# Kernel tuning notes

Hardware: AMD Instinct MI355X
Metric: run time of the kernel (lower is better)

The kernel has to match this reference:

```python
import jax, jax.numpy as jnp
import numpy as np

GRID_SIZE = 5
SPLINE_ORDER = 3

def _grid(in_features, dtype):
    # efficient-KAN default grid over [-1, 1], extended by spline_order knots each side
    h = 2.0 / GRID_SIZE
    g = jnp.arange(-SPLINE_ORDER, GRID_SIZE + SPLINE_ORDER + 1, dtype=dtype) * h - 1.0
    return jnp.broadcast_to(g, (in_features, g.shape[0]))  # (in, G+2k+1)

def _b_splines(x, grid):
    # x: (..., in) -> bases: (..., in, G+k) via Cox-de Boor recursion
    xk = x[..., None]
    bases = ((xk >= grid[:, :-1]) & (xk < grid[:, 1:])).astype(x.dtype)
    for k in range(1, SPLINE_ORDER + 1):
        left = (xk - grid[:, :-(k + 1)]) / (grid[:, k:-1] - grid[:, :-(k + 1)]) * bases[..., :-1]
        right = (grid[:, k + 1:] - xk) / (grid[:, k + 1:] - grid[:, 1:-k]) * bases[..., 1:]
        bases = left + right
    return bases

def _kan_linear(x, base_w, spline_w, scaler):
    # base branch: SiLU(x) @ W_base^T ; spline branch: einsum over B-spline basis
    grid = _grid(base_w.shape[1], x.dtype)
    bases = _b_splines(x, grid)                      # (..., in, G+k)
    scaled = spline_w * scaler[..., None]            # (out, in, G+k)
    base_out = jax.nn.silu(x) @ base_w.T
    spline_out = jnp.einsum('...ig,oig->...o', bases, scaled)
    return base_out + spline_out

def setup_inputs() -> dict:
    key = jax.random.key(0)
    ks = jax.random.split(key, 11)
    B, N, C, O = 2, 256, 64, 64
    GK = GRID_SIZE + SPLINE_ORDER
    return {
        'x': jax.random.normal(ks[0], (B, N, C), jnp.float32),
        'adj': jax.random.randint(ks[1], (B, N, N), 0, 2, jnp.int32),
        'fw_base': jax.random.normal(ks[2], (1, C), jnp.float32) * 0.1,
        'fw_spline': jax.random.normal(ks[3], (1, C, GK), jnp.float32) * 0.1,
        'fw_scaler': jax.random.normal(ks[4], (1, C), jnp.float32) * 0.1,
        'mw_base': jax.random.normal(ks[5], (O, C), jnp.float32) * 0.1,
        'mw_spline': jax.random.normal(ks[6], (O, C, GK), jnp.float32) * 0.1,
        'mw_scaler': jax.random.normal(ks[7], (O, C), jnp.float32) * 0.1,
        'uw_base': jax.random.normal(ks[8], (O, C + O), jnp.float32) * 0.1,
        'uw_spline': jax.random.normal(ks[9], (O, C + O, GK), jnp.float32) * 0.1,
        'uw_scaler': jax.random.normal(ks[10], (O, C + O), jnp.float32) * 0.1,
    }

def reference(x, adj, fw_base, fw_spline, fw_scaler, mw_base, mw_spline, mw_scaler, uw_base, uw_spline, uw_scaler):
    # r_ij = h_i - h_j : (B, N, N, C)
    r_ij = x[:, :, None, :] - x[:, None, :, :]
    energy = _kan_linear(r_ij, fw_base, fw_spline, fw_scaler)[..., 0]  # (B, N, N)
    energy = jnp.where(adj == 0, jnp.asarray(-1e9, energy.dtype), energy)
    alpha = jax.nn.softmax(energy, axis=-1)
    msg_val = _kan_linear(x, mw_base, mw_spline, mw_scaler)            # (B, N, O)
    aggr = jnp.einsum('bij,bjo->bio', alpha, msg_val)
    combined = jnp.concatenate([x, aggr], axis=-1)
    return _kan_linear(combined, uw_base, uw_spline, uw_scaler)
```

## Files before the change

### kernel.cpp

```cpp
#include <hip/hip_runtime.h>
#include <math.h>

#define NB 256
#define CH 64
#define OUTF 64
#define GK 8
#define UIN 128
#define KM (CH * 9)
#define KM4 (KM / 4)
#define KU (UIN * 9)
#define KU4 (KU / 4)

#define WS_MSG 0
#define WS_W2M 32768
#define WS_W2U 69632

__device__ __forceinline__ float silu(float v) {
    return v * __builtin_amdgcn_rcpf(1.0f + __expf(-v));
}

__device__ __forceinline__ void spline4(float r, int& d, float4& v) {
    float p = fmaf(r, 2.5f, 5.5f);
    float fd = floorf(p);
    d = (int)fd;
    float u = p - fd;
    if ((unsigned)d > 10u) d = 11;
    float um = 1.0f - u;
    float u2 = u * u, u3 = u2 * u;
    const float k6 = 1.0f / 6.0f;
    v.x = um * um * um * k6;
    v.y = (3.0f * u3 - 6.0f * u2 + 4.0f) * k6;
    v.z = (-3.0f * u3 + 3.0f * u2 + 3.0f * u + 1.0f) * k6;
    v.w = u3 * k6;
}

__global__ __launch_bounds__(256) void prep_kernel(
    const float* __restrict__ mwb, const float* __restrict__ mws,
    const float* __restrict__ mwsc,
    const float* __restrict__ uwb, const float* __restrict__ uws,
    const float* __restrict__ uwsc,
    float* __restrict__ ws) {
    int t = blockIdx.x * 256 + threadIdx.x;
    if (t < KM4 * OUTF) {
        int k4 = t >> 6, o = t & 63;
        float4 v;
#pragma unroll
        for (int kk = 0; kk < 4; ++kk) {
            int k = k4 * 4 + kk, c = k / 9, g = k - c * 9;
            ((float*)&v)[kk] = (g < 8)
                ? mws[(o * CH + c) * GK + g] * mwsc[o * CH + c]
                : mwb[o * CH + c];
        }
        ((float4*)(ws + WS_W2M))[t] = v;
        return;
    }
    int t2 = t - KM4 * OUTF;
    if (t2 < KU4 * OUTF) {
        int k4 = t2 >> 6, o = t2 & 63;
        float4 v;
#pragma unroll
        for (int kk = 0; kk < 4; ++kk) {
            int k = k4 * 4 + kk, c = k / 9, g = k - c * 9;
            ((float*)&v)[kk] = (g < 8)
                ? uws[(o * UIN + c) * GK + g] * uwsc[o * UIN + c]
                : uwb[o * UIN + c];
        }
        ((float4*)(ws + WS_W2U))[t2] = v;
    }
}

__global__ __launch_bounds__(256) void msg_kernel(
    const float* __restrict__ x, const float* __restrict__ w2m,
    float* __restrict__ msg) {
    const int row = blockIdx.x, tid = threadIdx.x;
    __shared__ __align__(16) float F[KM];
    __shared__ float part[4][OUTF];

    if (tid < CH) {
        float v = x[row * CH + tid];
#pragma unroll
        for (int g = 0; g < 8; ++g) F[tid * 9 + g] = 0.0f;
        F[tid * 9 + 8] = silu(v);
        int d; float4 vv; spline4(v, d, vv);
#pragma unroll
        for (int k = 0; k < 4; ++k) {
            int m = d - 3 + k;
            if ((unsigned)m < 8u) F[tid * 9 + m] = ((const float*)&vv)[k];
        }
    }
    __syncthreads();

    const int o = tid & 63, w = tid >> 6;
    const float4* W = (const float4*)w2m;
    const float4* Fv = (const float4*)F;
    float acc = 0.0f;
#pragma unroll 4
    for (int k4 = w * 36; k4 < w * 36 + 36; ++k4) {
        float4 f = Fv[k4];
        float4 wt = W[k4 * 64 + o];
        acc += f.x * wt.x + f.y * wt.y + f.z * wt.z + f.w * wt.w;
    }
    part[w][o] = acc;
    __syncthreads();
    if (tid < OUTF)
        msg[row * OUTF + tid] =
            part[0][tid] + part[1][tid] + part[2][tid] + part[3][tid];
}

__global__ __launch_bounds__(256, 2) void gat_kernel(
    const float* __restrict__ x,
    const int* __restrict__ adj,
    const float* __restrict__ fwb, const float* __restrict__ fws,
    const float* __restrict__ fwsc,
    const float* __restrict__ w2u,
    const float* __restrict__ msg,
    float* __restrict__ out) {
    const int b = blockIdx.x >> 8;
    const int i = blockIdx.x & 255;
    const int tid = threadIdx.x;

    __shared__ float4 cpad[CH][16];
    __shared__ float4 xi4[16];
    __shared__ float4 fb4[16];
    __shared__ float alpha[NB];
    __shared__ float comb[UIN];
    __shared__ __align__(16) float Fu[KU];
    __shared__ float4 part4[16][16];
    __shared__ float part[4][OUTF];
    __shared__ float wred[4];

    float4 xj[16];
    {
        const float4* xrow = (const float4*)(x + (b * NB + tid) * CH);
#pragma unroll
        for (int c4 = 0; c4 < 16; ++c4) xj[c4] = xrow[c4];
    }

    if (tid < 16) {
        float4 v = ((const float4*)(x + (b * NB + i) * CH))[tid];
        xi4[tid] = v;
        fb4[tid] = ((const float4*)fwb)[tid];
        ((float4*)comb)[tid] = v;
    }
#pragma unroll
    for (int e = tid; e < CH * 16; e += 256) {
        int c = e >> 4, dd = e & 15;
        float4 cf = make_float4(0.f, 0.f, 0.f, 0.f);
        if (dd <= 10) {
            float sc = fwsc[c];
            float w0 = 0.f, w1 = 0.f, w2 = 0.f, w3 = 0.f;
            int m0 = dd - 3;
            if ((unsigned)(m0 + 0) < 8u) w0 = fws[c * GK + m0 + 0] * sc;
            if ((unsigned)(m0 + 1) < 8u) w1 = fws[c * GK + m0 + 1] * sc;
            if ((unsigned)(m0 + 2) < 8u) w2 = fws[c * GK + m0 + 2] * sc;
            if ((unsigned)(m0 + 3) < 8u) w3 = fws[c * GK + m0 + 3] * sc;
            cf.x = (w0 + 4.0f * w1 + w2) * (1.0f / 6.0f);
            cf.y = (w2 - w0) * 0.5f;
            cf.z = (w0 - 2.0f * w1 + w2) * 0.5f;
            cf.w = (w3 - w0 + 3.0f * (w1 - w2)) * (1.0f / 6.0f);
        }
        cpad[c][dd] = cf;
    }
    __syncthreads();

    float e = 0.0f;
#pragma unroll
    for (int c4 = 0; c4 < 16; ++c4) {
        float4 xiv = xi4[c4];
        float4 fbv = fb4[c4];
        float4 xjv = xj[c4];
#pragma unroll
        for (int q = 0; q < 4; ++q) {
            float r = ((const float*)&xiv)[q] - ((const float*)&xjv)[q];
            float pp = fmaf(r, 2.5f, 5.5f);
            float fd = floorf(pp);
            int d = (int)fd;
            float u = pp - fd;
            if ((unsigned)d > 10u) d = 11;
            float4 cf = cpad[c4 * 4 + q][d];
            float t = fmaf(u, cf.w, cf.z);
            t = fmaf(u, t, cf.y);
            t = fmaf(u, t, cf.x);
            e += fmaf(silu(r), ((const float*)&fbv)[q], t);
        }
    }
    if (adj[(b * NB + i) * NB + tid] == 0) e = -1e9f;

    float mx = e;
#pragma unroll
    for (int off = 32; off > 0; off >>= 1)
        mx = fmaxf(mx, __shfl_xor(mx, off, 64));
    if ((tid & 63) == 0) wred[tid >> 6] = mx;
    __syncthreads();
    mx = fmaxf(fmaxf(wred[0], wred[1]), fmaxf(wred[2], wred[3]));
    float pexp = __expf(e - mx);
    float sw = pexp;
#pragma unroll
    for (int off = 32; off > 0; off >>= 1)
        sw += __shfl_xor(sw, off, 64);
    __syncthreads();
    if ((tid & 63) == 0) wred[tid >> 6] = sw;
    __syncthreads();
    float denom = wred[0] + wred[1] + wred[2] + wred[3];
    alpha[tid] = pexp * __builtin_amdgcn_rcpf(denom);
    __syncthreads();

    {
        const int o4 = tid & 15, seg = tid >> 4;
        const float4* msgb4 = (const float4*)(msg + (b * NB + seg * 16) * OUTF);
        float4 a = make_float4(0.f, 0.f, 0.f, 0.f);
#pragma unroll
        for (int jj = 0; jj < 16; ++jj) {
            float al = alpha[seg * 16 + jj];
            float4 mv = msgb4[jj * 16 + o4];
            a.x = fmaf(al, mv.x, a.x);
            a.y = fmaf(al, mv.y, a.y);
            a.z = fmaf(al, mv.z, a.z);
            a.w = fmaf(al, mv.w, a.w);
        }
        part4[seg][o4] = a;
    }
    __syncthreads();
    if (tid < OUTF) {
        const float* p = (const float*)part4;
        float s = 0.0f;
#pragma unroll
        for (int sg = 0; sg < 16; ++sg) s += p[sg * 64 + tid];
        comb[CH + tid] = s;
    }
    __syncthreads();

    if (tid < UIN) {
        float v = comb[tid];
#pragma unroll
        for (int g = 0; g < 8; ++g) Fu[tid * 9 + g] = 0.0f;
        Fu[tid * 9 + 8] = silu(v);
        int d; float4 vv; spline4(v, d, vv);
#pragma unroll
        for (int k = 0; k < 4; ++k) {
            int m = d - 3 + k;
            if ((unsigned)m < 8u) Fu[tid * 9 + m] = ((const float*)&vv)[k];
        }
    }
    __syncthreads();

    {
        const int o = tid & 63, w = tid >> 6;
        const float4* W = (const float4*)w2u;
        const float4* Fv = (const float4*)Fu;
        float acc = 0.0f;
#pragma unroll 4
        for (int k4 = w * 72; k4 < w * 72 + 72; ++k4) {
            float4 f = Fv[k4];
            float4 wt = W[k4 * 64 + o];
            acc += f.x * wt.x + f.y * wt.y + f.z * wt.z + f.w * wt.w;
        }
        part[w][o] = acc;
    }
    __syncthreads();
    if (tid < OUTF)
        out[(b * NB + i) * OUTF + tid] =
            part[0][tid] + part[1][tid] + part[2][tid] + part[3][tid];
}

extern "C" void kernel_launch(void* const* d_in, const int* in_sizes, int n_in,
                              void* d_out, int out_size, void* d_ws, size_t ws_size,
                              hipStream_t stream) {
    const float* x     = (const float*)d_in[0];
    const int*   adj   = (const int*)d_in[1];
    const float* fwb   = (const float*)d_in[2];
    const float* fws   = (const float*)d_in[3];
    const float* fwsc  = (const float*)d_in[4];
    const float* mwb   = (const float*)d_in[5];
    const float* mws   = (const float*)d_in[6];
    const float* mwsc  = (const float*)d_in[7];
    const float* uwb   = (const float*)d_in[8];
    const float* uws   = (const float*)d_in[9];
    const float* uwsc  = (const float*)d_in[10];
    float* out = (float*)d_out;
    float* ws = (float*)d_ws;

    const int BN = in_sizes[0] / CH;

    const int prep_threads = KM4 * OUTF + KU4 * OUTF;
    prep_kernel<<<(prep_threads + 255) / 256, 256, 0, stream>>>(
        mwb, mws, mwsc, uwb, uws, uwsc, ws);
    msg_kernel<<<BN, 256, 0, stream>>>(x, ws + WS_W2M, ws + WS_MSG);
    gat_kernel<<<BN, 256, 0, stream>>>(x, adj, fwb, fws, fwsc,
                                       ws + WS_W2U, ws + WS_MSG, out);
}
```

Measured before the change: 99.39 us.

## Process two query rows per block and precompute spline coefficient table in prep

Each msg and gat block now handles two rows, so the loaded xj neighbor rows, msg values, and w2u/w2m weight streams are reused across two outputs instead of being refetched per row. The cubic spline coefficient table for the energy KAN is computed once in the prep kernel and copied from workspace rather than rebuilt by every block. This halves the grid size (256 blocks for 512 rows) and raises register and shared-memory use per block, which may reduce occupancy and latency hiding.

```diff
diff --git a/kernel.cpp b/kernel.cpp
--- a/kernel.cpp
+++ b/kernel.cpp
@@ -14,6 +14,7 @@
 #define WS_MSG 0
 #define WS_W2M 32768
 #define WS_W2U 69632
+#define WS_CPAD 143360
 
 __device__ __forceinline__ float silu(float v) {
     return v * __builtin_amdgcn_rcpf(1.0f + __expf(-v));
@@ -39,6 +40,7 @@
     const float* __restrict__ mwsc,
     const float* __restrict__ uwb, const float* __restrict__ uws,
     const float* __restrict__ uwsc,
+    const float* __restrict__ fws, const float* __restrict__ fwsc,
     float* __restrict__ ws) {
     int t = blockIdx.x * 256 + threadIdx.x;
     if (t < KM4 * OUTF) {
@@ -66,85 +68,11 @@
                 : uwb[o * UIN + c];
         }
         ((float4*)(ws + WS_W2U))[t2] = v;
-    }
-}
-
-__global__ __launch_bounds__(256) void msg_kernel(
-    const float* __restrict__ x, const float* __restrict__ w2m,
-    float* __restrict__ msg) {
-    const int row = blockIdx.x, tid = threadIdx.x;
-    __shared__ __align__(16) float F[KM];
-    __shared__ float part[4][OUTF];
-
-    if (tid < CH) {
-        float v = x[row * CH + tid];
-#pragma unroll
-        for (int g = 0; g < 8; ++g) F[tid * 9 + g] = 0.0f;
-        F[tid * 9 + 8] = silu(v);
-        int d; float4 vv; spline4(v, d, vv);
-#pragma unroll
-        for (int k = 0; k < 4; ++k) {
-            int m = d - 3 + k;
-            if ((unsigned)m < 8u) F[tid * 9 + m] = ((const float*)&vv)[k];
-        }
-    }
-    __syncthreads();
-
-    const int o = tid & 63, w = tid >> 6;
-    const float4* W = (const float4*)w2m;
-    const float4* Fv = (const float4*)F;
-    float acc = 0.0f;
-#pragma unroll 4
-    for (int k4 = w * 36; k4 < w * 36 + 36; ++k4) {
-        float4 f = Fv[k4];
-        float4 wt = W[k4 * 64 + o];
-        acc += f.x * wt.x + f.y * wt.y + f.z * wt.z + f.w * wt.w;
-    }
-    part[w][o] = acc;
-    __syncthreads();
-    if (tid < OUTF)
-        msg[row * OUTF + tid] =
-            part[0][tid] + part[1][tid] + part[2][tid] + part[3][tid];
-}
-
-__global__ __launch_bounds__(256, 2) void gat_kernel(
-    const float* __restrict__ x,
-    const int* __restrict__ adj,
-    const float* __restrict__ fwb, const float* __restrict__ fws,
-    const float* __restrict__ fwsc,
-    const float* __restrict__ w2u,
-    const float* __restrict__ msg,
-    float* __restrict__ out) {
-    const int b = blockIdx.x >> 8;
-    const int i = blockIdx.x & 255;
-    const int tid = threadIdx.x;
-
-    __shared__ float4 cpad[CH][16];
-    __shared__ float4 xi4[16];
-    __shared__ float4 fb4[16];
-    __shared__ float alpha[NB];
-    __shared__ float comb[UIN];
-    __shared__ __align__(16) float Fu[KU];
-    __shared__ float4 part4[16][16];
-    __shared__ float part[4][OUTF];
-    __shared__ float wred[4];
-
-    float4 xj[16];
-    {
-        const float4* xrow = (const float4*)(x + (b * NB + tid) * CH);
-#pragma unroll
-        for (int c4 = 0; c4 < 16; ++c4) xj[c4] = xrow[c4];
-    }
-
-    if (tid < 16) {
-        float4 v = ((const float4*)(x + (b * NB + i) * CH))[tid];
-        xi4[tid] = v;
-        fb4[tid] = ((const float4*)fwb)[tid];
-        ((float4*)comb)[tid] = v;
-    }
-#pragma unroll
-    for (int e = tid; e < CH * 16; e += 256) {
-        int c = e >> 4, dd = e & 15;
+        return;
+    }
+    int t3 = t2 - KU4 * OUTF;
+    if (t3 < CH * 16) {
+        int c = t3 >> 4, dd = t3 & 15;
         float4 cf = make_float4(0.f, 0.f, 0.f, 0.f);
         if (dd <= 10) {
             float sc = fwsc[c];
@@ -159,87 +87,230 @@
             cf.z = (w0 - 2.0f * w1 + w2) * 0.5f;
             cf.w = (w3 - w0 + 3.0f * (w1 - w2)) * (1.0f / 6.0f);
         }
-        cpad[c][dd] = cf;
-    }
-    __syncthreads();
-
-    float e = 0.0f;
+        ((float4*)(ws + WS_CPAD))[t3] = cf;
+    }
+}
+
+__global__ __launch_bounds__(256) void msg_kernel(
+    const float* __restrict__ x, const float* __restrict__ w2m,
+    float* __restrict__ msg) {
+    const int r0 = blockIdx.x * 2, tid = threadIdx.x;
+    __shared__ __align__(16) float F0[KM];
+    __shared__ __align__(16) float F1[KM];
+    __shared__ float pa[4][OUTF];
+    __shared__ float pb[4][OUTF];
+
+    if (tid < 2 * CH) {
+        int rr = tid >> 6, c = tid & 63;
+        float* Fr = rr ? F1 : F0;
+        float v = x[(r0 + rr) * CH + c];
+#pragma unroll
+        for (int g = 0; g < 8; ++g) Fr[c * 9 + g] = 0.0f;
+        Fr[c * 9 + 8] = silu(v);
+        int d; float4 vv; spline4(v, d, vv);
+#pragma unroll
+        for (int k = 0; k < 4; ++k) {
+            int m = d - 3 + k;
+            if ((unsigned)m < 8u) Fr[c * 9 + m] = ((const float*)&vv)[k];
+        }
+    }
+    __syncthreads();
+
+    const int o = tid & 63, w = tid >> 6;
+    const float4* W = (const float4*)w2m;
+    const float4* Fv0 = (const float4*)F0;
+    const float4* Fv1 = (const float4*)F1;
+    float a0 = 0.0f, a1 = 0.0f;
+#pragma unroll 4
+    for (int k4 = w * 36; k4 < w * 36 + 36; ++k4) {
+        float4 f0 = Fv0[k4];
+        float4 f1 = Fv1[k4];
+        float4 wt = W[k4 * 64 + o];
+        a0 += f0.x * wt.x + f0.y * wt.y + f0.z * wt.z + f0.w * wt.w;
+        a1 += f1.x * wt.x + f1.y * wt.y + f1.z * wt.z + f1.w * wt.w;
+    }
+    pa[w][o] = a0;
+    pb[w][o] = a1;
+    __syncthreads();
+    if (tid < OUTF)
+        msg[r0 * OUTF + tid] = pa[0][tid] + pa[1][tid] + pa[2][tid] + pa[3][tid];
+    else if (tid < 2 * OUTF) {
+        int o2 = tid - OUTF;
+        msg[(r0 + 1) * OUTF + o2] = pb[0][o2] + pb[1][o2] + pb[2][o2] + pb[3][o2];
+    }
+}
+
+__global__ __launch_bounds__(256) void gat_kernel(
+    const float* __restrict__ x,
+    const int* __restrict__ adj,
+    const float* __restrict__ fwb,
+    const float* __restrict__ cpadg,
+    const float* __restrict__ w2u,
+    const float* __restrict__ msg,
+    float* __restrict__ out) {
+    const int b = blockIdx.x >> 7;
+    const int i0 = (blockIdx.x & 127) * 2;
+    const int i1 = i0 + 1;
+    const int tid = threadIdx.x;
+
+    __shared__ float4 cpad[CH][16];
+    __shared__ float4 xi0_4[16];
+    __shared__ float4 xi1_4[16];
+    __shared__ float4 fb4[16];
+    __shared__ float alpha0[NB];
+    __shared__ float alpha1[NB];
+    __shared__ float comb0[UIN];
+    __shared__ float comb1[UIN];
+    __shared__ __align__(16) float Fu0[KU];
+    __shared__ __align__(16) float Fu1[KU];
+    __shared__ float4 p4a[16][16];
+    __shared__ float4 p4b[16][16];
+    __shared__ float p2a[4][OUTF];
+    __shared__ float p2b[4][OUTF];
+    __shared__ float wredA[4], wredB[4];
+
+    float4 xj[16];
+    {
+        const float4* xrow = (const float4*)(x + (b * NB + tid) * CH);
+#pragma unroll
+        for (int c4 = 0; c4 < 16; ++c4) xj[c4] = xrow[c4];
+    }
+
+    if (tid < 16) {
+        float4 v = ((const float4*)(x + (b * NB + i0) * CH))[tid];
+        xi0_4[tid] = v;
+        ((float4*)comb0)[tid] = v;
+    } else if (tid < 32) {
+        float4 v = ((const float4*)(x + (b * NB + i1) * CH))[tid - 16];
+        xi1_4[tid - 16] = v;
+        ((float4*)comb1)[tid - 16] = v;
+    } else if (tid < 48) {
+        fb4[tid - 32] = ((const float4*)fwb)[tid - 32];
+    }
+    {
+        const float4* cp = (const float4*)cpadg;
+        float4* cds = (float4*)cpad;
+#pragma unroll
+        for (int k = 0; k < 4; ++k) cds[tid + k * 256] = cp[tid + k * 256];
+    }
+    __syncthreads();
+
+    float e0 = 0.0f, e1 = 0.0f;
 #pragma unroll
     for (int c4 = 0; c4 < 16; ++c4) {
-        float4 xiv = xi4[c4];
+        float4 xiv0 = xi0_4[c4];
+        float4 xiv1 = xi1_4[c4];
         float4 fbv = fb4[c4];
         float4 xjv = xj[c4];
 #pragma unroll
         for (int q = 0; q < 4; ++q) {
-            float r = ((const float*)&xiv)[q] - ((const float*)&xjv)[q];
-            float pp = fmaf(r, 2.5f, 5.5f);
-            float fd = floorf(pp);
-            int d = (int)fd;
-            float u = pp - fd;
-            if ((unsigned)d > 10u) d = 11;
-            float4 cf = cpad[c4 * 4 + q][d];
-            float t = fmaf(u, cf.w, cf.z);
-            t = fmaf(u, t, cf.y);
-            t = fmaf(u, t, cf.x);
-            e += fmaf(silu(r), ((const float*)&fbv)[q], t);
-        }
-    }
-    if (adj[(b * NB + i) * NB + tid] == 0) e = -1e9f;
-
-    float mx = e;
-#pragma unroll
-    for (int off = 32; off > 0; off >>= 1)
-        mx = fmaxf(mx, __shfl_xor(mx, off, 64));
-    if ((tid & 63) == 0) wred[tid >> 6] = mx;
-    __syncthreads();
-    mx = fmaxf(fmaxf(wred[0], wred[1]), fmaxf(wred[2], wred[3]));
-    float pexp = __expf(e - mx);
-    float sw = pexp;
-#pragma unroll
-    for (int off = 32; off > 0; off >>= 1)
-        sw += __shfl_xor(sw, off, 64);
-    __syncthreads();
-    if ((tid & 63) == 0) wred[tid >> 6] = sw;
-    __syncthreads();
-    float denom = wred[0] + wred[1] + wred[2] + wred[3];
-    alpha[tid] = pexp * __builtin_amdgcn_rcpf(denom);
+            float xq = ((const float*)&xjv)[q];
+            float fb = ((const float*)&fbv)[q];
+            {
+                float r = ((const float*)&xiv0)[q] - xq;
+                float pp = fmaf(r, 2.5f, 5.5f);
+                float fd = floorf(pp);
+                int d = (int)fd;
+                float u = pp - fd;
+                if ((unsigned)d > 10u) d = 11;
+                float4 cf = cpad[c4 * 4 + q][d];
+                float t = fmaf(u, cf.w, cf.z);
+                t = fmaf(u, t, cf.y);
+                t = fmaf(u, t, cf.x);
+                e0 += fmaf(silu(r), fb, t);
+            }
+            {
+                float r = ((const float*)&xiv1)[q] - xq;
+                float pp = fmaf(r, 2.5f, 5.5f);
+                float fd = floorf(pp);
+                int d = (int)fd;
+                float u = pp - fd;
+                if ((unsigned)d > 10u) d = 11;
+                float4 cf = cpad[c4 * 4 + q][d];
+                float t = fmaf(u, cf.w, cf.z);
+                t = fmaf(u, t, cf.y);
+                t = fmaf(u, t, cf.x);
+                e1 += fmaf(silu(r), fb, t);
+            }
+        }
+    }
+    if (adj[(b * NB + i0) * NB + tid] == 0) e0 = -1e9f;
+    if (adj[(b * NB + i1) * NB + tid] == 0) e1 = -1e9f;
+
+    float mx0 = e0, mx1 = e1;
+#pragma unroll
+    for (int off = 32; off > 0; off >>= 1) {
+        mx0 = fmaxf(mx0, __shfl_xor(mx0, off, 64));
+        mx1 = fmaxf(mx1, __shfl_xor(mx1, off, 64));
+    }
+    if ((tid & 63) == 0) { wredA[tid >> 6] = mx0; wredB[tid >> 6] = mx1; }
+    __syncthreads();
+    mx0 = fmaxf(fmaxf(wredA[0], wredA[1]), fmaxf(wredA[2], wredA[3]));
+    mx1 = fmaxf(fmaxf(wredB[0], wredB[1]), fmaxf(wredB[2], wredB[3]));
+    float p0 = __expf(e0 - mx0), p1 = __expf(e1 - mx1);
+    float s0 = p0, s1 = p1;
+#pragma unroll
+    for (int off = 32; off > 0; off >>= 1) {
+        s0 += __shfl_xor(s0, off, 64);
+        s1 += __shfl_xor(s1, off, 64);
+    }
+    __syncthreads();
+    if ((tid & 63) == 0) { wredA[tid >> 6] = s0; wredB[tid >> 6] = s1; }
+    __syncthreads();
+    float den0 = wredA[0] + wredA[1] + wredA[2] + wredA[3];
+    float den1 = wredB[0] + wredB[1] + wredB[2] + wredB[3];
+    alpha0[tid] = p0 * __builtin_amdgcn_rcpf(den0);
+    alpha1[tid] = p1 * __builtin_amdgcn_rcpf(den1);
     __syncthreads();
 
     {
         const int o4 = tid & 15, seg = tid >> 4;
         const float4* msgb4 = (const float4*)(msg + (b * NB + seg * 16) * OUTF);
-        float4 a = make_float4(0.f, 0.f, 0.f, 0.f);
+        float4 a0 = make_float4(0.f, 0.f, 0.f, 0.f);
+        float4 a1 = make_float4(0.f, 0.f, 0.f, 0.f);
 #pragma unroll
         for (int jj = 0; jj < 16; ++jj) {
-            float al = alpha[seg * 16 + jj];
+            float al0 = alpha0[seg * 16 + jj];
+            float al1 = alpha1[seg * 16 + jj];
             float4 mv = msgb4[jj * 16 + o4];
-            a.x = fmaf(al, mv.x, a.x);
-            a.y = fmaf(al, mv.y, a.y);
-            a.z = fmaf(al, mv.z, a.z);
-            a.w = fmaf(al, mv.w, a.w);
-        }
-        part4[seg][o4] = a;
+            a0.x = fmaf(al0, mv.x, a0.x); a0.y = fmaf(al0, mv.y, a0.y);
+            a0.z = fmaf(al0, mv.z, a0.z); a0.w = fmaf(al0, mv.w, a0.w);
+            a1.x = fmaf(al1, mv.x, a1.x); a1.y = fmaf(al1, mv.y, a1.y);
+            a1.z = fmaf(al1, mv.z, a1.z); a1.w = fmaf(al1, mv.w, a1.w);
+        }
+        p4a[seg][o4] = a0;
+        p4b[seg][o4] = a1;
     }
     __syncthreads();
     if (tid < OUTF) {
-        const float* p = (const float*)part4;
+        const float* p = (const float*)p4a;
         float s = 0.0f;
 #pragma unroll
         for (int sg = 0; sg < 16; ++sg) s += p[sg * 64 + tid];
-        comb[CH + tid] = s;
-    }
-    __syncthreads();
-
-    if (tid < UIN) {
-        float v = comb[tid];
-#pragma unroll
-        for (int g = 0; g < 8; ++g) Fu[tid * 9 + g] = 0.0f;
-        Fu[tid * 9 + 8] = silu(v);
+        comb0[CH + tid] = s;
+    } else if (tid < 2 * OUTF) {
+        const float* p = (const float*)p4b;
+        int o2 = tid - OUTF;
+        float s = 0.0f;
+#pragma unroll
+        for (int sg = 0; sg < 16; ++sg) s += p[sg * 64 + o2];
+        comb1[CH + o2] = s;
+    }
+    __syncthreads();
+
+    {
+        int rr = tid >> 7, c = tid & 127;
+        const float* cb = rr ? comb1 : comb0;
+        float* Fr = rr ? Fu1 : Fu0;
+        float v = cb[c];
+#pragma unroll
+        for (int g = 0; g < 8; ++g) Fr[c * 9 + g] = 0.0f;
+        Fr[c * 9 + 8] = silu(v);
         int d; float4 vv; spline4(v, d, vv);
 #pragma unroll
         for (int k = 0; k < 4; ++k) {
             int m = d - 3 + k;
-            if ((unsigned)m < 8u) Fu[tid * 9 + m] = ((const float*)&vv)[k];
+            if ((unsigned)m < 8u) Fr[c * 9 + m] = ((const float*)&vv)[k];
         }
     }
     __syncthreads();
@@ -247,20 +318,29 @@
     {
         const int o = tid & 63, w = tid >> 6;
         const float4* W = (const float4*)w2u;
-        const float4* Fv = (const float4*)Fu;
-        float acc = 0.0f;
+        const float4* Fv0 = (const float4*)Fu0;
+        const float4* Fv1 = (const float4*)Fu1;
+        float a0 = 0.0f, a1 = 0.0f;
 #pragma unroll 4
         for (int k4 = w * 72; k4 < w * 72 + 72; ++k4) {
-            float4 f = Fv[k4];
+            float4 f0 = Fv0[k4];
+            float4 f1 = Fv1[k4];
             float4 wt = W[k4 * 64 + o];
-            acc += f.x * wt.x + f.y * wt.y + f.z * wt.z + f.w * wt.w;
-        }
-        part[w][o] = acc;
+            a0 += f0.x * wt.x + f0.y * wt.y + f0.z * wt.z + f0.w * wt.w;
+            a1 += f1.x * wt.x + f1.y * wt.y + f1.z * wt.z + f1.w * wt.w;
+        }
+        p2a[w][o] = a0;
+        p2b[w][o] = a1;
     }
     __syncthreads();
     if (tid < OUTF)
-        out[(b * NB + i) * OUTF + tid] =
-            part[0][tid] + part[1][tid] + part[2][tid] + part[3][tid];
+        out[(b * NB + i0) * OUTF + tid] =
+            p2a[0][tid] + p2a[1][tid] + p2a[2][tid] + p2a[3][tid];
+    else if (tid < 2 * OUTF) {
+        int o2 = tid - OUTF;
+        out[(b * NB + i1) * OUTF + o2] =
+            p2b[0][o2] + p2b[1][o2] + p2b[2][o2] + p2b[3][o2];
+    }
 }
 
 extern "C" void kernel_launch(void* const* d_in, const int* in_sizes, int n_in,
@@ -282,10 +362,10 @@
 
     const int BN = in_sizes[0] / CH;
 
-    const int prep_threads = KM4 * OUTF + KU4 * OUTF;
+    const int prep_threads = KM4 * OUTF + KU4 * OUTF + CH * 16;
     prep_kernel<<<(prep_threads + 255) / 256, 256, 0, stream>>>(
-        mwb, mws, mwsc, uwb, uws, uwsc, ws);
-    msg_kernel<<<BN, 256, 0, stream>>>(x, ws + WS_W2M, ws + WS_MSG);
-    gat_kernel<<<BN, 256, 0, stream>>>(x, adj, fwb, fws, fwsc,
-                                       ws + WS_W2U, ws + WS_MSG, out);
-}
+        mwb, mws, mwsc, uwb, uws, uwsc, fws, fwsc, ws);
+    msg_kernel<<<BN / 2, 256, 0, stream>>>(x, ws + WS_W2M, ws + WS_MSG);
+    gat_kernel<<<BN / 2, 256, 0, stream>>>(x, adj, fwb, ws + WS_CPAD,
+                                           ws + WS_W2U, ws + WS_MSG, out);
+}
```

New measurement: 99.96 us. Within noise of the previous version (+0.6%).

## Fuse prep, message and attention kernels into one launch with grid barrier

Applied to the files above, without the earlier changes.

Merges the three kernels into a single persistent launch of 512 blocks. Each block computes its own message row directly from the raw spline weights, so the prepacked message matrix is no longer needed, and it packs its slice of the update weights. A hierarchical atomic grid barrier then publishes those results before the attention and update phases. This removes two kernel launches and their inter-kernel gaps. In exchange it relies on all 512 blocks being co-resident, since the spin barrier would deadlock otherwise, and it adds global atomic traffic and some redundant work.

```diff
diff --git a/kernel.cpp b/kernel.cpp
--- a/kernel.cpp
+++ b/kernel.cpp
@@ -6,14 +6,15 @@
 #define OUTF 64
 #define GK 8
 #define UIN 128
-#define KM (CH * 9)
-#define KM4 (KM / 4)
 #define KU (UIN * 9)
 #define KU4 (KU / 4)
 
 #define WS_MSG 0
-#define WS_W2M 32768
-#define WS_W2U 69632
+#define WS_W2U 32768
+
+__device__ int g_cnt[256];
+__device__ int g_sub;
+__device__ int g_epoch;
 
 __device__ __forceinline__ float silu(float v) {
     return v * __builtin_amdgcn_rcpf(1.0f + __expf(-v));
@@ -34,113 +35,47 @@
     v.w = u3 * k6;
 }
 
-__global__ __launch_bounds__(256) void prep_kernel(
+__global__ __launch_bounds__(256, 2) void fused_kernel(
+    const float* __restrict__ x,
+    const int* __restrict__ adj,
+    const float* __restrict__ fwb, const float* __restrict__ fws,
+    const float* __restrict__ fwsc,
     const float* __restrict__ mwb, const float* __restrict__ mws,
     const float* __restrict__ mwsc,
     const float* __restrict__ uwb, const float* __restrict__ uws,
     const float* __restrict__ uwsc,
-    float* __restrict__ ws) {
-    int t = blockIdx.x * 256 + threadIdx.x;
-    if (t < KM4 * OUTF) {
-        int k4 = t >> 6, o = t & 63;
-        float4 v;
-#pragma unroll
-        for (int kk = 0; kk < 4; ++kk) {
-            int k = k4 * 4 + kk, c = k / 9, g = k - c * 9;
-            ((float*)&v)[kk] = (g < 8)
-                ? mws[(o * CH + c) * GK + g] * mwsc[o * CH + c]
-                : mwb[o * CH + c];
-        }
-        ((float4*)(ws + WS_W2M))[t] = v;
-        return;
-    }
-    int t2 = t - KM4 * OUTF;
-    if (t2 < KU4 * OUTF) {
-        int k4 = t2 >> 6, o = t2 & 63;
-        float4 v;
-#pragma unroll
-        for (int kk = 0; kk < 4; ++kk) {
-            int k = k4 * 4 + kk, c = k / 9, g = k - c * 9;
-            ((float*)&v)[kk] = (g < 8)
-                ? uws[(o * UIN + c) * GK + g] * uwsc[o * UIN + c]
-                : uwb[o * UIN + c];
-        }
-        ((float4*)(ws + WS_W2U))[t2] = v;
-    }
-}
-
-__global__ __launch_bounds__(256) void msg_kernel(
-    const float* __restrict__ x, const float* __restrict__ w2m,
-    float* __restrict__ msg) {
-    const int row = blockIdx.x, tid = threadIdx.x;
-    __shared__ __align__(16) float F[KM];
-    __shared__ float part[4][OUTF];
-
-    if (tid < CH) {
-        float v = x[row * CH + tid];
-#pragma unroll
-        for (int g = 0; g < 8; ++g) F[tid * 9 + g] = 0.0f;
-        F[tid * 9 + 8] = silu(v);
-        int d; float4 vv; spline4(v, d, vv);
-#pragma unroll
-        for (int k = 0; k < 4; ++k) {
-            int m = d - 3 + k;
-            if ((unsigned)m < 8u) F[tid * 9 + m] = ((const float*)&vv)[k];
-        }
-    }
-    __syncthreads();
-
-    const int o = tid & 63, w = tid >> 6;
-    const float4* W = (const float4*)w2m;
-    const float4* Fv = (const float4*)F;
-    float acc = 0.0f;
-#pragma unroll 4
-    for (int k4 = w * 36; k4 < w * 36 + 36; ++k4) {
-        float4 f = Fv[k4];
-        float4 wt = W[k4 * 64 + o];
-        acc += f.x * wt.x + f.y * wt.y + f.z * wt.z + f.w * wt.w;
-    }
-    part[w][o] = acc;
-    __syncthreads();
-    if (tid < OUTF)
-        msg[row * OUTF + tid] =
-            part[0][tid] + part[1][tid] + part[2][tid] + part[3][tid];
-}
-
-__global__ __launch_bounds__(256, 2) void gat_kernel(
-    const float* __restrict__ x,
-    const int* __restrict__ adj,
-    const float* __restrict__ fwb, const float* __restrict__ fws,
-    const float* __restrict__ fwsc,
-    const float* __restrict__ w2u,
-    const float* __restrict__ msg,
+    float* __restrict__ ws,
     float* __restrict__ out) {
-    const int b = blockIdx.x >> 8;
-    const int i = blockIdx.x & 255;
     const int tid = threadIdx.x;
+    const int r = blockIdx.x;
+    const int b = r >> 8, i = r & 255;
 
     __shared__ float4 cpad[CH][16];
     __shared__ float4 xi4[16];
     __shared__ float4 fb4[16];
-    __shared__ float alpha[NB];
-    __shared__ float comb[UIN];
-    __shared__ __align__(16) float Fu[KU];
-    __shared__ float4 part4[16][16];
-    __shared__ float part[4][OUTF];
-    __shared__ float wred[4];
-
-    float4 xj[16];
-    {
-        const float4* xrow = (const float4*)(x + (b * NB + tid) * CH);
-#pragma unroll
-        for (int c4 = 0; c4 < 16; ++c4) xj[c4] = xrow[c4];
-    }
-
-    if (tid < 16) {
-        float4 v = ((const float4*)(x + (b * NB + i) * CH))[tid];
-        xi4[tid] = v;
-        fb4[tid] = ((const float4*)fwb)[tid];
-        ((float4*)comb)[tid] = v;
+    __shared__ __align__(16) char pool[11392];
+
+    float* F2   = (float*)pool;
+    float* pmsg = (float*)(pool + 4096);
+    float*  alpha = (float*)pool;
+    float*  comb  = (float*)(pool + 1024);
+    float*  Fu    = (float*)(pool + 1536);
+    float4* part4 = (float4*)(pool + 6144);
+    float*  p2    = (float*)(pool + 10240);
+    float*  wred  = (float*)(pool + 11264);
+
+    if (tid < CH) {
+        float v = x[r * CH + tid];
+        float* Fc = F2 + tid * 16;
+#pragma unroll
+        for (int g = 0; g < 8; ++g) Fc[g] = 0.0f;
+        Fc[8] = silu(v);
+        int d; float4 vv; spline4(v, d, vv);
+#pragma unroll
+        for (int k = 0; k < 4; ++k) {
+            int m = d - 3 + k;
+            if ((unsigned)m < 8u) Fc[m] = ((const float*)&vv)[k];
+        }
     }
 #pragma unroll
     for (int e = tid; e < CH * 16; e += 256) {
@@ -161,9 +96,101 @@
         }
         cpad[c][dd] = cf;
     }
-    __syncthreads();
-
-    float e = 0.0f;
+    if (tid < 16) {
+        xi4[tid] = ((const float4*)(x + (b * NB + i) * CH))[tid];
+    } else if (tid < 32) {
+        fb4[tid - 16] = ((const float4*)fwb)[tid - 16];
+    }
+    if (tid < 36) {
+        int item = r * 36 + tid;
+        int k4 = item >> 6, o = item & 63;
+        float4 v;
+#pragma unroll
+        for (int kk = 0; kk < 4; ++kk) {
+            int k = k4 * 4 + kk, c = k / 9, g = k - c * 9;
+            ((float*)&v)[kk] = (g < 8)
+                ? uws[(o * UIN + c) * GK + g] * uwsc[o * UIN + c]
+                : uwb[o * UIN + c];
+        }
+        ((float4*)(ws + WS_W2U))[item] = v;
+    }
+    __syncthreads();
+
+    {
+        const int o = tid & 63, cw = tid >> 6, c0 = cw * 16;
+        const float4* mws4 = (const float4*)mws;
+        float acc = 0.0f;
+#pragma unroll
+        for (int gq = 0; gq < 4; ++gq) {
+            int c = c0 + gq * 4;
+            float4 scv = *(const float4*)(mwsc + o * CH + c);
+            float4 bbv = *(const float4*)(mwb + o * CH + c);
+#pragma unroll
+            for (int q = 0; q < 4; ++q) {
+                int cc = c + q;
+                float4 w0 = mws4[(o * CH + cc) * 2];
+                float4 w1 = mws4[(o * CH + cc) * 2 + 1];
+                const float* Fc = F2 + cc * 16;
+                float4 f0 = *(const float4*)Fc;
+                float4 f1 = *(const float4*)(Fc + 4);
+                float dot = w0.x * f0.x + w0.y * f0.y + w0.z * f0.z
+                          + w0.w * f0.w + w1.x * f1.x + w1.y * f1.y
+                          + w1.z * f1.z + w1.w * f1.w;
+                acc = fmaf(((const float*)&scv)[q], dot, acc);
+                acc = fmaf(((const float*)&bbv)[q], Fc[8], acc);
+            }
+        }
+        pmsg[cw * 64 + o] = acc;
+    }
+    __syncthreads();
+    if (tid < OUTF)
+        ws[WS_MSG + r * OUTF + tid] =
+            pmsg[tid] + pmsg[64 + tid] + pmsg[128 + tid] + pmsg[192 + tid];
+
+    float4 xj[16];
+    {
+        const float4* xrow = (const float4*)(x + (b * NB + tid) * CH);
+#pragma unroll
+        for (int c4 = 0; c4 < 16; ++c4) xj[c4] = xrow[c4];
+    }
+    int adjv = adj[(b * NB + i) * NB + tid];
+
+    __syncthreads();
+    if (tid == 0) {
+        int ep = __hip_atomic_load(&g_epoch, __ATOMIC_RELAXED,
+                                   __HIP_MEMORY_SCOPE_AGENT);
+        int k = (r & 7) * 32;
+        int gsz = (int)(gridDim.x >> 3);
+        int prev = __hip_atomic_fetch_add(&g_cnt[k], 1, __ATOMIC_ACQ_REL,
+                                          __HIP_MEMORY_SCOPE_AGENT);
+        bool released = false;
+        if (prev == gsz - 1) {
+            __hip_atomic_store(&g_cnt[k], 0, __ATOMIC_RELAXED,
+                               __HIP_MEMORY_SCOPE_AGENT);
+            int p2v = __hip_atomic_fetch_add(&g_sub, 1, __ATOMIC_ACQ_REL,
+                                             __HIP_MEMORY_SCOPE_AGENT);
+            if (p2v == 7) {
+                __hip_atomic_store(&g_sub, 0, __ATOMIC_RELAXED,
+                                   __HIP_MEMORY_SCOPE_AGENT);
+                __hip_atomic_store(&g_epoch, ep + 1, __ATOMIC_RELEASE,
+                                   __HIP_MEMORY_SCOPE_AGENT);
+                released = true;
+            }
+        }
+        if (!released) {
+            for (int it = 0; it < (1 << 20); ++it) {
+                if (__hip_atomic_load(&g_epoch, __ATOMIC_ACQUIRE,
+                                      __HIP_MEMORY_SCOPE_AGENT) != ep) break;
+                __builtin_amdgcn_s_sleep(16);
+            }
+        }
+    }
+    __syncthreads();
+    __threadfence();
+
+    if (tid < 16) ((float4*)comb)[tid] = xi4[tid];
+
+    float e0 = 0.0f;
 #pragma unroll
     for (int c4 = 0; c4 < 16; ++c4) {
         float4 xiv = xi4[c4];
@@ -171,8 +198,8 @@
         float4 xjv = xj[c4];
 #pragma unroll
         for (int q = 0; q < 4; ++q) {
-            float r = ((const float*)&xiv)[q] - ((const float*)&xjv)[q];
-            float pp = fmaf(r, 2.5f, 5.5f);
+            float rr = ((const float*)&xiv)[q] - ((const float*)&xjv)[q];
+            float pp = fmaf(rr, 2.5f, 5.5f);
             float fd = floorf(pp);
             int d = (int)fd;
             float u = pp - fd;
@@ -181,19 +208,19 @@
             float t = fmaf(u, cf.w, cf.z);
             t = fmaf(u, t, cf.y);
             t = fmaf(u, t, cf.x);
-            e += fmaf(silu(r), ((const float*)&fbv)[q], t);
-        }
-    }
-    if (adj[(b * NB + i) * NB + tid] == 0) e = -1e9f;
-
-    float mx = e;
+            e0 += fmaf(silu(rr), ((const float*)&fbv)[q], t);
+        }
+    }
+    if (adjv == 0) e0 = -1e9f;
+
+    float mx = e0;
 #pragma unroll
     for (int off = 32; off > 0; off >>= 1)
         mx = fmaxf(mx, __shfl_xor(mx, off, 64));
     if ((tid & 63) == 0) wred[tid >> 6] = mx;
     __syncthreads();
     mx = fmaxf(fmaxf(wred[0], wred[1]), fmaxf(wred[2], wred[3]));
-    float pexp = __expf(e - mx);
+    float pexp = __expf(e0 - mx);
     float sw = pexp;
 #pragma unroll
     for (int off = 32; off > 0; off >>= 1)
@@ -207,7 +234,8 @@
 
     {
         const int o4 = tid & 15, seg = tid >> 4;
-        const float4* msgb4 = (const float4*)(msg + (b * NB + seg * 16) * OUTF);
+        const float4* msgb4 =
+            (const float4*)(ws + WS_MSG + (b * NB + seg * 16) * OUTF);
         float4 a = make_float4(0.f, 0.f, 0.f, 0.f);
 #pragma unroll
         for (int jj = 0; jj < 16; ++jj) {
@@ -218,7 +246,7 @@
             a.z = fmaf(al, mv.z, a.z);
             a.w = fmaf(al, mv.w, a.w);
         }
-        part4[seg][o4] = a;
+        part4[seg * 16 + o4] = a;
     }
     __syncthreads();
     if (tid < OUTF) {
@@ -246,7 +274,7 @@
 
     {
         const int o = tid & 63, w = tid >> 6;
-        const float4* W = (const float4*)w2u;
+        const float4* W = (const float4*)(ws + WS_W2U);
         const float4* Fv = (const float4*)Fu;
         float acc = 0.0f;
 #pragma unroll 4
@@ -255,12 +283,12 @@
             float4 wt = W[k4 * 64 + o];
             acc += f.x * wt.x + f.y * wt.y + f.z * wt.z + f.w * wt.w;
         }
-        part[w][o] = acc;
+        p2[w * 64 + o] = acc;
     }
     __syncthreads();
     if (tid < OUTF)
-        out[(b * NB + i) * OUTF + tid] =
-            part[0][tid] + part[1][tid] + part[2][tid] + part[3][tid];
+        out[r * OUTF + tid] =
+            p2[tid] + p2[64 + tid] + p2[128 + tid] + p2[192 + tid];
 }
 
 extern "C" void kernel_launch(void* const* d_in, const int* in_sizes, int n_in,
@@ -282,10 +310,7 @@
 
     const int BN = in_sizes[0] / CH;
 
-    const int prep_threads = KM4 * OUTF + KU4 * OUTF;
-    prep_kernel<<<(prep_threads + 255) / 256, 256, 0, stream>>>(
-        mwb, mws, mwsc, uwb, uws, uwsc, ws);
-    msg_kernel<<<BN, 256, 0, stream>>>(x, ws + WS_W2M, ws + WS_MSG);
-    gat_kernel<<<BN, 256, 0, stream>>>(x, adj, fwb, fws, fwsc,
-                                       ws + WS_W2U, ws + WS_MSG, out);
+    fused_kernel<<<BN, 256, 0, stream>>>(x, adj, fwb, fws, fwsc,
+                                         mwb, mws, mwsc, uwb, uws, uwsc,
+                                         ws, out);
 }
```

Measured after the change: 186.0 us. 87.1% more time.

## Fold weight prep into msg kernel and precompute spline coefficients once

Applied to the files above, without the earlier changes.

Removes the separate prep kernel launch. Its work is spread across the 512 msg blocks: each block packs 36 float4 of the update weights and 2 entries of the energy-spline coefficient table into the workspace. The message KAN now reads the raw mws/mwsc/mwb weights directly, exploiting the sparse 16-wide basis layout. The gat kernel copies the precomputed coefficient table instead of recomputing it in every block. This saves one launch and redundant per-block coefficient work, at the cost of less coalesced weight reads in the message matmul.

```diff
diff --git a/kernel.cpp b/kernel.cpp
--- a/kernel.cpp
+++ b/kernel.cpp
@@ -6,14 +6,12 @@
 #define OUTF 64
 #define GK 8
 #define UIN 128
-#define KM (CH * 9)
-#define KM4 (KM / 4)
 #define KU (UIN * 9)
 #define KU4 (KU / 4)
 
 #define WS_MSG 0
-#define WS_W2M 32768
-#define WS_W2U 69632
+#define WS_W2U 32768
+#define WS_CPAD 106496
 
 __device__ __forceinline__ float silu(float v) {
     return v * __builtin_amdgcn_rcpf(1.0f + __expf(-v));
@@ -34,29 +32,34 @@
     v.w = u3 * k6;
 }
 
-__global__ __launch_bounds__(256) void prep_kernel(
+__global__ __launch_bounds__(256) void msg_kernel(
+    const float* __restrict__ x,
     const float* __restrict__ mwb, const float* __restrict__ mws,
     const float* __restrict__ mwsc,
     const float* __restrict__ uwb, const float* __restrict__ uws,
     const float* __restrict__ uwsc,
+    const float* __restrict__ fws, const float* __restrict__ fwsc,
     float* __restrict__ ws) {
-    int t = blockIdx.x * 256 + threadIdx.x;
-    if (t < KM4 * OUTF) {
-        int k4 = t >> 6, o = t & 63;
-        float4 v;
-#pragma unroll
-        for (int kk = 0; kk < 4; ++kk) {
-            int k = k4 * 4 + kk, c = k / 9, g = k - c * 9;
-            ((float*)&v)[kk] = (g < 8)
-                ? mws[(o * CH + c) * GK + g] * mwsc[o * CH + c]
-                : mwb[o * CH + c];
-        }
-        ((float4*)(ws + WS_W2M))[t] = v;
-        return;
-    }
-    int t2 = t - KM4 * OUTF;
-    if (t2 < KU4 * OUTF) {
-        int k4 = t2 >> 6, o = t2 & 63;
+    const int r = blockIdx.x, tid = threadIdx.x;
+    __shared__ __align__(16) float F2[CH * 16];
+    __shared__ float pmsg[4][OUTF];
+
+    if (tid < CH) {
+        float v = x[r * CH + tid];
+        float* Fc = F2 + tid * 16;
+#pragma unroll
+        for (int g = 0; g < 8; ++g) Fc[g] = 0.0f;
+        Fc[8] = silu(v);
+        int d; float4 vv; spline4(v, d, vv);
+#pragma unroll
+        for (int k = 0; k < 4; ++k) {
+            int m = d - 3 + k;
+            if ((unsigned)m < 8u) Fc[m] = ((const float*)&vv)[k];
+        }
+    }
+    if (tid >= 64 && tid < 100) {
+        int item = r * 36 + (tid - 64);
+        int k4 = item >> 6, o = item & 63;
         float4 v;
 #pragma unroll
         for (int kk = 0; kk < 4; ++kk) {
@@ -65,85 +68,10 @@
                 ? uws[(o * UIN + c) * GK + g] * uwsc[o * UIN + c]
                 : uwb[o * UIN + c];
         }
-        ((float4*)(ws + WS_W2U))[t2] = v;
-    }
-}
-
-__global__ __launch_bounds__(256) void msg_kernel(
-    const float* __restrict__ x, const float* __restrict__ w2m,
-    float* __restrict__ msg) {
-    const int row = blockIdx.x, tid = threadIdx.x;
-    __shared__ __align__(16) float F[KM];
-    __shared__ float part[4][OUTF];
-
-    if (tid < CH) {
-        float v = x[row * CH + tid];
-#pragma unroll
-        for (int g = 0; g < 8; ++g) F[tid * 9 + g] = 0.0f;
-        F[tid * 9 + 8] = silu(v);
-        int d; float4 vv; spline4(v, d, vv);
-#pragma unroll
-        for (int k = 0; k < 4; ++k) {
-            int m = d - 3 + k;
-            if ((unsigned)m < 8u) F[tid * 9 + m] = ((const float*)&vv)[k];
-        }
-    }
-    __syncthreads();
-
-    const int o = tid & 63, w = tid >> 6;
-    const float4* W = (const float4*)w2m;
-    const float4* Fv = (const float4*)F;
-    float acc = 0.0f;
-#pragma unroll 4
-    for (int k4 = w * 36; k4 < w * 36 + 36; ++k4) {
-        float4 f = Fv[k4];
-        float4 wt = W[k4 * 64 + o];
-        acc += f.x * wt.x + f.y * wt.y + f.z * wt.z + f.w * wt.w;
-    }
-    part[w][o] = acc;
-    __syncthreads();
-    if (tid < OUTF)
-        msg[row * OUTF + tid] =
-            part[0][tid] + part[1][tid] + part[2][tid] + part[3][tid];
-}
-
-__global__ __launch_bounds__(256, 2) void gat_kernel(
-    const float* __restrict__ x,
-    const int* __restrict__ adj,
-    const float* __restrict__ fwb, const float* __restrict__ fws,
-    const float* __restrict__ fwsc,
-    const float* __restrict__ w2u,
-    const float* __restrict__ msg,
-    float* __restrict__ out) {
-    const int b = blockIdx.x >> 8;
-    const int i = blockIdx.x & 255;
-    const int tid = threadIdx.x;
-
-    __shared__ float4 cpad[CH][16];
-    __shared__ float4 xi4[16];
-    __shared__ float4 fb4[16];
-    __shared__ float alpha[NB];
-    __shared__ float comb[UIN];
-    __shared__ __align__(16) float Fu[KU];
-    __shared__ float4 part4[16][16];
-    __shared__ float part[4][OUTF];
-    __shared__ float wred[4];
-
-    float4 xj[16];
-    {
-        const float4* xrow = (const float4*)(x + (b * NB + tid) * CH);
-#pragma unroll
-        for (int c4 = 0; c4 < 16; ++c4) xj[c4] = xrow[c4];
-    }
-
-    if (tid < 16) {
-        float4 v = ((const float4*)(x + (b * NB + i) * CH))[tid];
-        xi4[tid] = v;
-        fb4[tid] = ((const float4*)fwb)[tid];
-        ((float4*)comb)[tid] = v;
-    }
-#pragma unroll
-    for (int e = tid; e < CH * 16; e += 256) {
+        ((float4*)(ws + WS_W2U))[item] = v;
+    }
+    if (tid >= 100 && tid < 102) {
+        int e = r * 2 + (tid - 100);
         int c = e >> 4, dd = e & 15;
         float4 cf = make_float4(0.f, 0.f, 0.f, 0.f);
         if (dd <= 10) {
@@ -159,7 +87,83 @@
             cf.z = (w0 - 2.0f * w1 + w2) * 0.5f;
             cf.w = (w3 - w0 + 3.0f * (w1 - w2)) * (1.0f / 6.0f);
         }
-        cpad[c][dd] = cf;
+        ((float4*)(ws + WS_CPAD))[e] = cf;
+    }
+    __syncthreads();
+
+    {
+        const int o = tid & 63, cw = tid >> 6, c0 = cw * 16;
+        const float4* mws4 = (const float4*)mws;
+        float acc = 0.0f;
+#pragma unroll
+        for (int gq = 0; gq < 4; ++gq) {
+            int c = c0 + gq * 4;
+            float4 scv = *(const float4*)(mwsc + o * CH + c);
+            float4 bbv = *(const float4*)(mwb + o * CH + c);
+#pragma unroll
+            for (int q = 0; q < 4; ++q) {
+                int cc = c + q;
+                float4 w0 = mws4[(o * CH + cc) * 2];
+                float4 w1 = mws4[(o * CH + cc) * 2 + 1];
+                const float* Fc = F2 + cc * 16;
+                float4 f0 = *(const float4*)Fc;
+                float4 f1 = *(const float4*)(Fc + 4);
+                float dot = w0.x * f0.x + w0.y * f0.y + w0.z * f0.z
+                          + w0.w * f0.w + w1.x * f1.x + w1.y * f1.y
+                          + w1.z * f1.z + w1.w * f1.w;
+                acc = fmaf(((const float*)&scv)[q], dot, acc);
+                acc = fmaf(((const float*)&bbv)[q], Fc[8], acc);
+            }
+        }
+        pmsg[cw][o] = acc;
+    }
+    __syncthreads();
+    if (tid < OUTF)
+        ws[WS_MSG + r * OUTF + tid] =
+            pmsg[0][tid] + pmsg[1][tid] + pmsg[2][tid] + pmsg[3][tid];
+}
+
+__global__ __launch_bounds__(256, 2) void gat_kernel(
+    const float* __restrict__ x,
+    const int* __restrict__ adj,
+    const float* __restrict__ fwb,
+    const float* __restrict__ cpadg,
+    const float* __restrict__ w2u,
+    const float* __restrict__ msg,
+    float* __restrict__ out) {
+    const int b = blockIdx.x >> 8;
+    const int i = blockIdx.x & 255;
+    const int tid = threadIdx.x;
+
+    __shared__ float4 cpad[CH][16];
+    __shared__ float4 xi4[16];
+    __shared__ float4 fb4[16];
+    __shared__ float alpha[NB];
+    __shared__ float comb[UIN];
+    __shared__ __align__(16) float Fu[KU];
+    __shared__ float4 part4[16][16];
+    __shared__ float part[4][OUTF];
+    __shared__ float wred[4];
+
+    float4 xj[16];
+    {
+        const float4* xrow = (const float4*)(x + (b * NB + tid) * CH);
+#pragma unroll
+        for (int c4 = 0; c4 < 16; ++c4) xj[c4] = xrow[c4];
+    }
+
+    if (tid < 16) {
+        float4 v = ((const float4*)(x + (b * NB + i) * CH))[tid];
+        xi4[tid] = v;
+        ((float4*)comb)[tid] = v;
+    } else if (tid < 32) {
+        fb4[tid - 16] = ((const float4*)fwb)[tid - 16];
+    }
+    {
+        const float4* cp = (const float4*)cpadg;
+        float4* cds = (float4*)cpad;
+#pragma unroll
+        for (int k = 0; k < 4; ++k) cds[tid + k * 256] = cp[tid + k * 256];
     }
     __syncthreads();
 
@@ -282,10 +286,8 @@
 
     const int BN = in_sizes[0] / CH;
 
-    const int prep_threads = KM4 * OUTF + KU4 * OUTF;
-    prep_kernel<<<(prep_threads + 255) / 256, 256, 0, stream>>>(
-        mwb, mws, mwsc, uwb, uws, uwsc, ws);
-    msg_kernel<<<BN, 256, 0, stream>>>(x, ws + WS_W2M, ws + WS_MSG);
-    gat_kernel<<<BN, 256, 0, stream>>>(x, adj, fwb, fws, fwsc,
+    msg_kernel<<<BN, 256, 0, stream>>>(x, mwb, mws, mwsc, uwb, uws, uwsc,
+                                       fws, fwsc, ws);
+    gat_kernel<<<BN, 256, 0, stream>>>(x, adj, fwb, ws + WS_CPAD,
                                        ws + WS_W2U, ws + WS_MSG, out);
 }
```

Result: slower. 105.4 us (+6.0%).
